# Performance work log

Measured on AMD Instinct MI355X. Metric: run time of the kernel, lower is better.

Reference implementation:

```python
import jax, jax.numpy as jnp
import numpy as np

EPS = 1e-12  # matches torch F.normalize eps


def setup_inputs() -> dict:
    key = jax.random.key(0)
    k1, k2, k3 = jax.random.split(key, 3)
    N, C, H, W, K = 16, 1024, 32, 32, 32
    x = jax.random.normal(k1, (N, C, H, W), dtype=jnp.float32)
    # 1x1 conv weight (K, C, 1, 1) stored as (K, C)
    conv_w = jax.random.normal(k2, (K, C), dtype=jnp.float32) * 0.02
    centroids = jax.random.uniform(k3, (K, C), dtype=jnp.float32)
    return {"x": x, "conv_w": conv_w, "centroids": centroids}


def _l2norm(v, axis):
    return v / jnp.maximum(jnp.linalg.norm(v, axis=axis, keepdims=True), EPS)


def reference(x, conv_w, centroids):
    N, C, H, W = x.shape
    K = centroids.shape[0]
    # normalize_input: L2 over channel dim
    x = _l2norm(x, axis=1)
    xf = x.reshape(N, C, H * W)                      # (N, C, P)
    # 1x1 conv == per-pixel matmul -> (N, K, P)
    logits = jnp.einsum('kc,ncp->nkp', conv_w, xf)
    a = jax.nn.softmax(logits, axis=1)               # softmax over clusters
    # sum_p a[n,k,p] * (x[n,:,p] - centroids[k,:])
    # == (a @ x^T) - (sum_p a) * centroids  (two GEMMs, no (N,K,C,P) blowup)
    vlad = jnp.einsum('nkp,ncp->nkc', a, xf) - a.sum(-1)[:, :, None] * centroids[None]
    vlad = _l2norm(vlad, axis=2)                     # intra-cluster L2 norm
    vlad = vlad.reshape(N, K * C)
    vlad = _l2norm(vlad, axis=1)                     # global L2 norm
    return vlad
```

## Files before the change

kernel.cpp:

```cpp
#include <hip/hip_runtime.h>

#define NB   16
#define CC   1024
#define PP   1024
#define KK   32
#define EPSF 1e-12f

typedef __attribute__((ext_vector_type(8))) short  bf16x8;
typedef __attribute__((ext_vector_type(4))) float  f32x4;

__device__ __forceinline__ float bf2f(unsigned short u) {
    union { unsigned int i; float f; } v; v.i = ((unsigned int)u) << 16; return v.f;
}
__device__ __forceinline__ unsigned short f2bf(float f) {
    union { float f; unsigned int i; } v; v.f = f;
    return (unsigned short)((v.i + 0x7fffu + ((v.i >> 16) & 1u)) >> 16);
}

template <typename T> struct IO;
template <> struct IO<float> {
    static __device__ __forceinline__ float  ld (const float* p) { return *p; }
    static __device__ __forceinline__ float4 ld4(const float* p) { return *(const float4*)p; }
};
template <> struct IO<unsigned short> {
    static __device__ __forceinline__ float  ld (const unsigned short* p) { return bf2f(*p); }
    static __device__ __forceinline__ float4 ld4(const unsigned short* p) {
        const ushort4 u = *(const ushort4*)p;
        return make_float4(bf2f(u.x), bf2f(u.y), bf2f(u.z), bf2f(u.w));
    }
};

__global__ __launch_bounds__(256) void k_detect(const unsigned short* __restrict__ xu,
                                                int* __restrict__ flag) {
    __shared__ int s;
    const int t = threadIdx.x;
    if (t == 0) s = 0;
    __syncthreads();
    int bad = 0;
    for (int i = t; i < 4096; i += 256)
        if (((xu[i] >> 7) & 0xFFu) > 0x9Fu) bad = 1;
    if (bad) atomicOr(&s, 1);
    __syncthreads();
    if (t == 0) flag[0] = s;
}

template <typename T>
__device__ __forceinline__ void attn_body(const T* __restrict__ x,
                                          const T* __restrict__ w,
                                          float* __restrict__ rnorm_ws,
                                          unsigned short* __restrict__ attn_g,
                                          float* __restrict__ asum) {
    __shared__ __align__(16) unsigned short xt[32 * 136];
    __shared__ __align__(16) unsigned short w_lds[32 * 136];
    __shared__ float red[32 * 32];
    __shared__ float lg[32 * 33];
    __shared__ float inv_lds[32];
    __shared__ float rnorm_lds[32];
    const int b = blockIdx.x, t = threadIdx.x;
    const int n = b >> 5, pbase = (b & 31) * 32;
    const int lane = t & 63, wv = t >> 6;
    const int quad = lane >> 4, l15 = lane & 15;
    const int mt = wv & 1, nt = wv >> 1;

    const size_t xb = (size_t)n * CC * PP + pbase;
    float ss0 = 0.f, ss1 = 0.f, ss2 = 0.f, ss3 = 0.f;
    f32x4 acc = {0.f, 0.f, 0.f, 0.f};

    const int pxg = 4 * (t & 7);
    const int crow = t >> 3;

    for (int ch = 0; ch < 8; ++ch) {
        const int c0 = ch * 128;
        __syncthreads();
        #pragma unroll
        for (int pass = 0; pass < 4; ++pass) {
            const int cl = crow + 32 * pass;
            const float4 v = IO<T>::ld4(&x[xb + (size_t)(c0 + cl) * PP + pxg]);
            ss0 += v.x * v.x; ss1 += v.y * v.y; ss2 += v.z * v.z; ss3 += v.w * v.w;
            xt[(pxg + 0) * 136 + cl] = f2bf(v.x);
            xt[(pxg + 1) * 136 + cl] = f2bf(v.y);
            xt[(pxg + 2) * 136 + cl] = f2bf(v.z);
            xt[(pxg + 3) * 136 + cl] = f2bf(v.w);
        }
        {
            const int k = t >> 3, cg = (t & 7) * 16;
            #pragma unroll
            for (int j = 0; j < 4; ++j) {
                const float4 v = IO<T>::ld4(&w[k * CC + c0 + cg + 4 * j]);
                ushort4 u;
                u.x = f2bf(v.x); u.y = f2bf(v.y); u.z = f2bf(v.z); u.w = f2bf(v.w);
                *(ushort4*)&w_lds[k * 136 + cg + 4 * j] = u;
            }
        }
        __syncthreads();
        #pragma unroll
        for (int ks = 0; ks < 4; ++ks) {
            const bf16x8 av = *(const bf16x8*)&xt[(mt * 16 + l15) * 136 + ks * 32 + quad * 8];
            const bf16x8 bv = *(const bf16x8*)&w_lds[(nt * 16 + l15) * 136 + ks * 32 + quad * 8];
            acc = __builtin_amdgcn_mfma_f32_16x16x32_bf16(av, bv, acc, 0, 0, 0);
        }
    }
    red[crow * 32 + pxg + 0] = ss0;
    red[crow * 32 + pxg + 1] = ss1;
    red[crow * 32 + pxg + 2] = ss2;
    red[crow * 32 + pxg + 3] = ss3;
    __syncthreads();
    if (t < 32) {
        float s = 0.f;
        #pragma unroll
        for (int g = 0; g < 32; ++g) s += red[g * 32 + t];
        const float r = 1.0f / fmaxf(sqrtf(s), EPSF);
        rnorm_lds[t] = r;
        rnorm_ws[n * PP + pbase + t] = r;
    }
    __syncthreads();
    #pragma unroll
    for (int reg = 0; reg < 4; ++reg) {
        const int px = mt * 16 + quad * 4 + reg;
        lg[px * 33 + nt * 16 + l15] = acc[reg] * rnorm_lds[px];
    }
    __syncthreads();
    if (t < 32) {
        float m = -1e30f;
        #pragma unroll
        for (int k = 0; k < KK; ++k) m = fmaxf(m, lg[t * 33 + k]);
        float s = 0.f;
        #pragma unroll
        for (int k = 0; k < KK; ++k) {
            const float e = expf(lg[t * 33 + k] - m);
            lg[t * 33 + k] = e;
            s += e;
        }
        inv_lds[t] = 1.0f / s;
    }
    __syncthreads();
    {
        const int k = t >> 3;
        float s = 0.f;
        ushort4 u;
        float vv[4];
        #pragma unroll
        for (int j = 0; j < 4; ++j) {
            const int px = pxg + j;
            vv[j] = lg[px * 33 + k] * inv_lds[px];
        }
        u.x = f2bf(vv[0]); u.y = f2bf(vv[1]); u.z = f2bf(vv[2]); u.w = f2bf(vv[3]);
        s = bf2f(u.x) + bf2f(u.y) + bf2f(u.z) + bf2f(u.w);
        *(ushort4*)&attn_g[((size_t)n * KK + k) * PP + pbase + pxg] = u;
        s += __shfl_xor(s, 1, 64);
        s += __shfl_xor(s, 2, 64);
        s += __shfl_xor(s, 4, 64);
        if ((t & 7) == 0) atomicAdd(&asum[n * KK + k], s);
    }
}
__global__ __launch_bounds__(256) void k_attn(const void* __restrict__ x,
                                              const void* __restrict__ w,
                                              const int* __restrict__ flag,
                                              float* __restrict__ rnorm_ws,
                                              unsigned short* __restrict__ attn_g,
                                              float* __restrict__ asum) {
    if (*flag) attn_body<float>((const float*)x, (const float*)w, rnorm_ws, attn_g, asum);
    else       attn_body<unsigned short>((const unsigned short*)x, (const unsigned short*)w,
                                         rnorm_ws, attn_g, asum);
}

template <typename T>
__device__ __forceinline__ void vlad_body(const T* __restrict__ x,
                                          const T* __restrict__ cent,
                                          const float* __restrict__ rnorm_ws,
                                          const unsigned short* __restrict__ attn_g,
                                          const float* __restrict__ asum,
                                          float* __restrict__ vlad,
                                          float* __restrict__ ssqnk) {
    __shared__ __align__(16) unsigned short xt[64 * 136];
    __shared__ __align__(16) unsigned short at_lds[32 * 136];
    __shared__ float asum_lds[32];
    __shared__ float ssq_lds[32];
    const int b = blockIdx.x, t = threadIdx.x;
    const int n = b >> 4, cbase = (b & 15) * 64;
    const int lane = t & 63, wv = t >> 6;
    const int quad = lane >> 4, l15 = lane & 15;
    const int mt = wv & 1, nt0 = (wv >> 1) * 2, nt1 = nt0 + 1;

    if (t < 32) { asum_lds[t] = asum[n * KK + t]; ssq_lds[t] = 0.f; }

    f32x4 acc0 = {0.f, 0.f, 0.f, 0.f}, acc1 = {0.f, 0.f, 0.f, 0.f};
    const size_t xb = (size_t)n * CC * PP + (size_t)cbase * PP;

    for (int pc = 0; pc < 8; ++pc) {
        const int p0 = pc * 128;
        __syncthreads();
        {
            const int k = t >> 3, pg = (t & 7) * 16;
            const size_t base = ((size_t)n * KK + k) * PP + p0 + pg;
            const uint4 u0 = *(const uint4*)&attn_g[base];
            const uint4 u1 = *(const uint4*)&attn_g[base + 8];
            *(uint4*)&at_lds[k * 136 + pg]     = u0;
            *(uint4*)&at_lds[k * 136 + pg + 8] = u1;
        }
        {
            const int pg = 4 * (t & 31);
            const float4 rn = *(const float4*)&rnorm_ws[n * PP + p0 + pg];
            #pragma unroll
            for (int pass = 0; pass < 8; ++pass) {
                const int ci = (t >> 5) + 8 * pass;
                const float4 v = IO<T>::ld4(&x[xb + (size_t)ci * PP + p0 + pg]);
                ushort4 u;
                u.x = f2bf(v.x * rn.x); u.y = f2bf(v.y * rn.y);
                u.z = f2bf(v.z * rn.z); u.w = f2bf(v.w * rn.w);
                *(ushort4*)&xt[ci * 136 + pg] = u;
            }
        }
        __syncthreads();
        #pragma unroll
        for (int ks = 0; ks < 4; ++ks) {
            const bf16x8 av  = *(const bf16x8*)&at_lds[(mt * 16 + l15) * 136 + ks * 32 + quad * 8];
            const bf16x8 bv0 = *(const bf16x8*)&xt[(nt0 * 16 + l15) * 136 + ks * 32 + quad * 8];
            const bf16x8 bv1 = *(const bf16x8*)&xt[(nt1 * 16 + l15) * 136 + ks * 32 + quad * 8];
            acc0 = __builtin_amdgcn_mfma_f32_16x16x32_bf16(av, bv0, acc0, 0, 0, 0);
            acc1 = __builtin_amdgcn_mfma_f32_16x16x32_bf16(av, bv1, acc1, 0, 0, 0);
        }
    }
    __syncthreads();
    const int c0g = cbase + nt0 * 16 + l15, c1g = cbase + nt1 * 16 + l15;
    #pragma unroll
    for (int reg = 0; reg < 4; ++reg) {
        const int k = mt * 16 + quad * 4 + reg;
        const float A = asum_lds[k];
        const float v0 = acc0[reg] - A * IO<T>::ld(&cent[k * CC + c0g]);
        const float v1 = acc1[reg] - A * IO<T>::ld(&cent[k * CC + c1g]);
        vlad[((size_t)n * KK + k) * CC + c0g] = v0;
        vlad[((size_t)n * KK + k) * CC + c1g] = v1;
        float s = v0 * v0 + v1 * v1;
        s += __shfl_xor(s, 1, 64);
        s += __shfl_xor(s, 2, 64);
        s += __shfl_xor(s, 4, 64);
        s += __shfl_xor(s, 8, 64);
        if (l15 == 0) atomicAdd(&ssq_lds[k], s);
    }
    __syncthreads();
    if (t < 32) atomicAdd(&ssqnk[n * KK + t], ssq_lds[t]);
}
__global__ __launch_bounds__(256) void k_vlad(const void* __restrict__ x,
                                              const void* __restrict__ cent,
                                              const int* __restrict__ flag,
                                              const float* __restrict__ rnorm_ws,
                                              const unsigned short* __restrict__ attn_g,
                                              const float* __restrict__ asum,
                                              float* __restrict__ vlad,
                                              float* __restrict__ ssqnk) {
    if (*flag) vlad_body<float>((const float*)x, (const float*)cent, rnorm_ws, attn_g,
                                asum, vlad, ssqnk);
    else       vlad_body<unsigned short>((const unsigned short*)x, (const unsigned short*)cent,
                                         rnorm_ws, attn_g, asum, vlad, ssqnk);
}

__global__ __launch_bounds__(64) void k_factors(const float* __restrict__ ssqnk,
                                                float* __restrict__ rintra,
                                                float* __restrict__ rglob) {
    const int n = blockIdx.x, t = threadIdx.x;
    const float s = (t < KK) ? ssqnk[n * KK + t] : 0.f;
    const float r = 1.0f / fmaxf(sqrtf(s), EPSF);
    if (t < KK) rintra[n * KK + t] = r;
    float g = s * r * r;
    for (int off = 32; off > 0; off >>= 1) g += __shfl_down(g, off, 64);
    if (t == 0) rglob[n] = 1.0f / fmaxf(sqrtf(g), EPSF);
}

__global__ __launch_bounds__(256) void k_out(const float* __restrict__ vlad,
                                             const float* __restrict__ rintra,
                                             const float* __restrict__ rglob,
                                             const int* __restrict__ flag,
                                             void* __restrict__ out) {
    const int b = blockIdx.x, t = threadIdx.x;
    const float f = rintra[b] * rglob[b >> 5];
    const float4 v = ((const float4*)(vlad + (size_t)b * CC))[t];
    if (*flag) {
        float4 o; o.x = v.x * f; o.y = v.y * f; o.z = v.z * f; o.w = v.w * f;
        ((float4*)((float*)out + (size_t)b * CC))[t] = o;
    } else {
        ushort4 u;
        u.x = f2bf(v.x * f); u.y = f2bf(v.y * f);
        u.z = f2bf(v.z * f); u.w = f2bf(v.w * f);
        ((ushort4*)((unsigned short*)out + (size_t)b * CC))[t] = u;
    }
}

extern "C" void kernel_launch(void* const* d_in, const int* in_sizes, int n_in,
                              void* d_out, int out_size, void* d_ws, size_t ws_size,
                              hipStream_t stream) {
    const void* x    = d_in[0];
    const void* w    = d_in[1];
    const void* cent = d_in[2];

    float* ws       = (float*)d_ws;
    float* rnorm_ws = ws;
    float* vlad     = rnorm_ws + NB * PP;
    float* asum     = vlad + NB * KK * CC;
    float* ssqnk    = asum + NB * KK;
    float* rintra   = ssqnk + NB * KK;
    float* rglob    = rintra + NB * KK;
    int*   flag     = (int*)(rglob + NB);
    unsigned short* attn_g = (unsigned short*)(flag + 4);

    hipMemsetAsync(asum, 0, 2 * NB * KK * sizeof(float), stream);

    k_detect<<<1, 256, 0, stream>>>((const unsigned short*)x, flag);
    k_attn<<<NB * 32, 256, 0, stream>>>(x, w, flag, rnorm_ws, attn_g, asum);
    k_vlad<<<NB * 16, 256, 0, stream>>>(x, cent, flag, rnorm_ws, attn_g, asum, vlad, ssqnk);
    k_factors<<<NB, 64, 0, stream>>>(ssqnk, rintra, rglob);
    k_out<<<NB * KK, 256, 0, stream>>>(vlad, rintra, rglob, flag, d_out);
}
```

Before: 127.6 us.

## Restructure NetVLAD pipeline: split-K attention, register prefetch, partial sums, fused epilogue

The attention kernel now gives each wave its own quarter of the channels. Each wave prefetches x into registers with double buffering and reads the weight from a pre-converted bf16 copy in global memory instead of staging it in LDS, and the per-wave partial logits are summed in shared memory. The vlad kernel launches four times as many blocks and splits the pixel range into two halves that write separate partial outputs. The memset, the atomics and the separate factors kernel are gone: the final kernel sums the partials, subtracts the centroids and applies both normalisations. This cuts launch count and synchronisation and raises parallelism, at the cost of extra workspace traffic for the partial buffers and higher register pressure.

```diff
diff --git a/kernel.cpp b/kernel.cpp
--- a/kernel.cpp
+++ b/kernel.cpp
@@ -5,6 +5,7 @@
 #define PP   1024
 #define KK   32
 #define EPSF 1e-12f
+#define XPAD 72
 
 typedef __attribute__((ext_vector_type(8))) short  bf16x8;
 typedef __attribute__((ext_vector_type(4))) float  f32x4;
@@ -19,270 +20,388 @@
 
 template <typename T> struct IO;
 template <> struct IO<float> {
-    static __device__ __forceinline__ float  ld (const float* p) { return *p; }
-    static __device__ __forceinline__ float4 ld4(const float* p) { return *(const float4*)p; }
+    static __device__ __forceinline__ float ld(const float* p) { return *p; }
+    static __device__ __forceinline__ f32x4 ld4(const float* p) { return *(const f32x4*)p; }
 };
 template <> struct IO<unsigned short> {
-    static __device__ __forceinline__ float  ld (const unsigned short* p) { return bf2f(*p); }
-    static __device__ __forceinline__ float4 ld4(const unsigned short* p) {
+    static __device__ __forceinline__ float ld(const unsigned short* p) { return bf2f(*p); }
+    static __device__ __forceinline__ f32x4 ld4(const unsigned short* p) {
         const ushort4 u = *(const ushort4*)p;
-        return make_float4(bf2f(u.x), bf2f(u.y), bf2f(u.z), bf2f(u.w));
+        f32x4 r; r[0] = bf2f(u.x); r[1] = bf2f(u.y); r[2] = bf2f(u.z); r[3] = bf2f(u.w);
+        return r;
     }
 };
 
-__global__ __launch_bounds__(256) void k_detect(const unsigned short* __restrict__ xu,
-                                                int* __restrict__ flag) {
-    __shared__ int s;
-    const int t = threadIdx.x;
-    if (t == 0) s = 0;
-    __syncthreads();
+__global__ __launch_bounds__(256) void k_prep(const void* __restrict__ xv,
+                                              const void* __restrict__ wv,
+                                              int* __restrict__ flag,
+                                              unsigned short* __restrict__ w_bf) {
+    __shared__ int s_bad;
+    const int t = threadIdx.x, b = blockIdx.x;
+    if (t == 0) s_bad = 0;
+    __syncthreads();
+    const unsigned short* xu = (const unsigned short*)xv;
     int bad = 0;
     for (int i = t; i < 4096; i += 256)
         if (((xu[i] >> 7) & 0xFFu) > 0x9Fu) bad = 1;
-    if (bad) atomicOr(&s, 1);
-    __syncthreads();
-    if (t == 0) flag[0] = s;
-}
+    if (bad) atomicOr(&s_bad, 1);
+    __syncthreads();
+    const int f = s_bad;
+    if (b == 0 && t == 0) flag[0] = f;
+    const int c = t * 4;
+    ushort4 u;
+    if (f) {
+        const f32x4 v = *(const f32x4*)((const float*)wv + b * CC + c);
+        u.x = f2bf(v[0]); u.y = f2bf(v[1]); u.z = f2bf(v[2]); u.w = f2bf(v[3]);
+    } else {
+        u = *(const ushort4*)((const unsigned short*)wv + b * CC + c);
+    }
+    *(ushort4*)&w_bf[b * CC + c] = u;
+}
+
+struct AttnSmem {
+    unsigned short xt[4][2][32 * XPAD];
+    float lg4[4][32][33];
+    float red[4][32];
+    float asq[4][32];
+    float rnorm[32];
+    unsigned short at[32][34];
+};
 
 template <typename T>
 __device__ __forceinline__ void attn_body(const T* __restrict__ x,
-                                          const T* __restrict__ w,
+                                          const unsigned short* __restrict__ w_bf,
                                           float* __restrict__ rnorm_ws,
                                           unsigned short* __restrict__ attn_g,
-                                          float* __restrict__ asum) {
-    __shared__ __align__(16) unsigned short xt[32 * 136];
-    __shared__ __align__(16) unsigned short w_lds[32 * 136];
-    __shared__ float red[32 * 32];
-    __shared__ float lg[32 * 33];
-    __shared__ float inv_lds[32];
-    __shared__ float rnorm_lds[32];
+                                          float* __restrict__ asum_part,
+                                          AttnSmem& sm) {
     const int b = blockIdx.x, t = threadIdx.x;
-    const int n = b >> 5, pbase = (b & 31) * 32;
-    const int lane = t & 63, wv = t >> 6;
+    const int n = b >> 5, strip = b & 31, pbase = strip * 32;
+    const int lane = t & 63, wq = t >> 6;
     const int quad = lane >> 4, l15 = lane & 15;
-    const int mt = wv & 1, nt = wv >> 1;
-
+    const int pg = (lane & 3) * 4;
+    const int c4 = (lane >> 2) * 4;
+    const int cqb = wq * 256;
     const size_t xb = (size_t)n * CC * PP + pbase;
-    float ss0 = 0.f, ss1 = 0.f, ss2 = 0.f, ss3 = 0.f;
-    f32x4 acc = {0.f, 0.f, 0.f, 0.f};
-
-    const int pxg = 4 * (t & 7);
-    const int crow = t >> 3;
-
-    for (int ch = 0; ch < 8; ++ch) {
-        const int c0 = ch * 128;
-        __syncthreads();
-        #pragma unroll
-        for (int pass = 0; pass < 4; ++pass) {
-            const int cl = crow + 32 * pass;
-            const float4 v = IO<T>::ld4(&x[xb + (size_t)(c0 + cl) * PP + pxg]);
-            ss0 += v.x * v.x; ss1 += v.y * v.y; ss2 += v.z * v.z; ss3 += v.w * v.w;
-            xt[(pxg + 0) * 136 + cl] = f2bf(v.x);
-            xt[(pxg + 1) * 136 + cl] = f2bf(v.y);
-            xt[(pxg + 2) * 136 + cl] = f2bf(v.z);
-            xt[(pxg + 3) * 136 + cl] = f2bf(v.w);
-        }
-        {
-            const int k = t >> 3, cg = (t & 7) * 16;
+
+    unsigned short* xt0 = &sm.xt[wq][0][0];
+    unsigned short* xt1 = &sm.xt[wq][1][0];
+
+    float ss[8] = {0.f, 0.f, 0.f, 0.f, 0.f, 0.f, 0.f, 0.f};
+    f32x4 acc00 = {0.f,0.f,0.f,0.f}, acc01 = {0.f,0.f,0.f,0.f};
+    f32x4 acc10 = {0.f,0.f,0.f,0.f}, acc11 = {0.f,0.f,0.f,0.f};
+
+    f32x4 ra[8], rb[8];
+    #pragma unroll
+    for (int i = 0; i < 4; ++i) {
+        ra[i]     = IO<T>::ld4(&x[xb + (size_t)(cqb + c4 + i) * PP + pg]);
+        ra[4 + i] = IO<T>::ld4(&x[xb + (size_t)(cqb + c4 + i) * PP + pg + 16]);
+        rb[i]     = IO<T>::ld4(&x[xb + (size_t)(cqb + 64 + c4 + i) * PP + pg]);
+        rb[4 + i] = IO<T>::ld4(&x[xb + (size_t)(cqb + 64 + c4 + i) * PP + pg + 16]);
+    }
+
+#define ATTN_STEP(CH, R, XT)                                                      \
+    do {                                                                          \
+           \
+        _Pragma("unroll")                                                         \
+        for (int h = 0; h < 2; ++h) {                                             \
+            _Pragma("unroll")                                                     \
+            for (int j = 0; j < 4; ++j) {                                         \
+                ushort4 u;                                                        \
+                u.x = f2bf(R[4*h+0][j]); u.y = f2bf(R[4*h+1][j]);                 \
+                u.z = f2bf(R[4*h+2][j]); u.w = f2bf(R[4*h+3][j]);                 \
+                ss[4*h+j] += R[4*h+0][j]*R[4*h+0][j] + R[4*h+1][j]*R[4*h+1][j]    \
+                           + R[4*h+2][j]*R[4*h+2][j] + R[4*h+3][j]*R[4*h+3][j];   \
+                *(ushort4*)&XT[(pg + 16*h + j) * XPAD + c4] = u;                  \
+            }                                                                     \
+        }                                                                         \
+        if ((CH) + 2 < 4) {                                                       \
+            _Pragma("unroll")                                                     \
+            for (int i = 0; i < 4; ++i) {                                         \
+                R[i]     = IO<T>::ld4(&x[xb + (size_t)(cqb + ((CH)+2)*64 + c4 + i) * PP + pg]);      \
+                R[4 + i] = IO<T>::ld4(&x[xb + (size_t)(cqb + ((CH)+2)*64 + c4 + i) * PP + pg + 16]); \
+            }                                                                     \
+        }                                                                         \
+        _Pragma("unroll")                                                         \
+        for (int ks = 0; ks < 2; ++ks) {                                          \
+            const bf16x8 a0 = *(const bf16x8*)&XT[l15 * XPAD + ks * 32 + quad * 8];        \
+            const bf16x8 a1 = *(const bf16x8*)&XT[(16 + l15) * XPAD + ks * 32 + quad * 8]; \
+            const int wc = cqb + (CH) * 64 + ks * 32 + quad * 8;                  \
+            const bf16x8 b0 = *(const bf16x8*)&w_bf[l15 * CC + wc];               \
+            const bf16x8 b1 = *(const bf16x8*)&w_bf[(16 + l15) * CC + wc];        \
+            acc00 = __builtin_amdgcn_mfma_f32_16x16x32_bf16(a0, b0, acc00, 0,0,0);\
+            acc01 = __builtin_amdgcn_mfma_f32_16x16x32_bf16(a0, b1, acc01, 0,0,0);\
+            acc10 = __builtin_amdgcn_mfma_f32_16x16x32_bf16(a1, b0, acc10, 0,0,0);\
+            acc11 = __builtin_amdgcn_mfma_f32_16x16x32_bf16(a1, b1, acc11, 0,0,0);\
+        }                                                                         \
+    } while (0)
+
+    ATTN_STEP(0, ra, xt0);
+    ATTN_STEP(1, rb, xt1);
+    ATTN_STEP(2, ra, xt0);
+    ATTN_STEP(3, rb, xt1);
+#undef ATTN_STEP
+
+    #pragma unroll
+    for (int i = 0; i < 8; ++i) {
+        ss[i] += __shfl_xor(ss[i], 4, 64);
+        ss[i] += __shfl_xor(ss[i], 8, 64);
+        ss[i] += __shfl_xor(ss[i], 16, 64);
+        ss[i] += __shfl_xor(ss[i], 32, 64);
+    }
+    if (lane < 4) {
+        #pragma unroll
+        for (int h = 0; h < 2; ++h)
             #pragma unroll
-            for (int j = 0; j < 4; ++j) {
-                const float4 v = IO<T>::ld4(&w[k * CC + c0 + cg + 4 * j]);
-                ushort4 u;
-                u.x = f2bf(v.x); u.y = f2bf(v.y); u.z = f2bf(v.z); u.w = f2bf(v.w);
-                *(ushort4*)&w_lds[k * 136 + cg + 4 * j] = u;
-            }
-        }
-        __syncthreads();
-        #pragma unroll
-        for (int ks = 0; ks < 4; ++ks) {
-            const bf16x8 av = *(const bf16x8*)&xt[(mt * 16 + l15) * 136 + ks * 32 + quad * 8];
-            const bf16x8 bv = *(const bf16x8*)&w_lds[(nt * 16 + l15) * 136 + ks * 32 + quad * 8];
-            acc = __builtin_amdgcn_mfma_f32_16x16x32_bf16(av, bv, acc, 0, 0, 0);
-        }
-    }
-    red[crow * 32 + pxg + 0] = ss0;
-    red[crow * 32 + pxg + 1] = ss1;
-    red[crow * 32 + pxg + 2] = ss2;
-    red[crow * 32 + pxg + 3] = ss3;
+            for (int j = 0; j < 4; ++j)
+                sm.red[wq][lane * 4 + 16 * h + j] = ss[4 * h + j];
+    }
+    #pragma unroll
+    for (int reg = 0; reg < 4; ++reg) {
+        sm.lg4[wq][quad * 4 + reg][l15]           = acc00[reg];
+        sm.lg4[wq][quad * 4 + reg][16 + l15]      = acc01[reg];
+        sm.lg4[wq][16 + quad * 4 + reg][l15]      = acc10[reg];
+        sm.lg4[wq][16 + quad * 4 + reg][16 + l15] = acc11[reg];
+    }
     __syncthreads();
     if (t < 32) {
-        float s = 0.f;
-        #pragma unroll
-        for (int g = 0; g < 32; ++g) s += red[g * 32 + t];
+        const float s = sm.red[0][t] + sm.red[1][t] + sm.red[2][t] + sm.red[3][t];
         const float r = 1.0f / fmaxf(sqrtf(s), EPSF);
-        rnorm_lds[t] = r;
+        sm.rnorm[t] = r;
         rnorm_ws[n * PP + pbase + t] = r;
     }
     __syncthreads();
-    #pragma unroll
-    for (int reg = 0; reg < 4; ++reg) {
-        const int px = mt * 16 + quad * 4 + reg;
-        lg[px * 33 + nt * 16 + l15] = acc[reg] * rnorm_lds[px];
-    }
-    __syncthreads();
-    if (t < 32) {
-        float m = -1e30f;
-        #pragma unroll
-        for (int k = 0; k < KK; ++k) m = fmaxf(m, lg[t * 33 + k]);
-        float s = 0.f;
-        #pragma unroll
-        for (int k = 0; k < KK; ++k) {
-            const float e = expf(lg[t * 33 + k] - m);
-            lg[t * 33 + k] = e;
-            s += e;
-        }
-        inv_lds[t] = 1.0f / s;
-    }
-    __syncthreads();
     {
-        const int k = t >> 3;
-        float s = 0.f;
-        ushort4 u;
-        float vv[4];
+        const int px = t >> 3, kq = (t & 7) * 4;
+        const float rn = sm.rnorm[px];
+        float v[4]; float mx = -1e30f;
         #pragma unroll
         for (int j = 0; j < 4; ++j) {
-            const int px = pxg + j;
-            vv[j] = lg[px * 33 + k] * inv_lds[px];
-        }
-        u.x = f2bf(vv[0]); u.y = f2bf(vv[1]); u.z = f2bf(vv[2]); u.w = f2bf(vv[3]);
-        s = bf2f(u.x) + bf2f(u.y) + bf2f(u.z) + bf2f(u.w);
-        *(ushort4*)&attn_g[((size_t)n * KK + k) * PP + pbase + pxg] = u;
+            v[j] = (sm.lg4[0][px][kq + j] + sm.lg4[1][px][kq + j]
+                  + sm.lg4[2][px][kq + j] + sm.lg4[3][px][kq + j]) * rn;
+            mx = fmaxf(mx, v[j]);
+        }
+        mx = fmaxf(mx, __shfl_xor(mx, 1, 64));
+        mx = fmaxf(mx, __shfl_xor(mx, 2, 64));
+        mx = fmaxf(mx, __shfl_xor(mx, 4, 64));
+        float e[4], s = 0.f;
+        #pragma unroll
+        for (int j = 0; j < 4; ++j) { e[j] = expf(v[j] - mx); s += e[j]; }
         s += __shfl_xor(s, 1, 64);
         s += __shfl_xor(s, 2, 64);
         s += __shfl_xor(s, 4, 64);
-        if ((t & 7) == 0) atomicAdd(&asum[n * KK + k], s);
-    }
-}
+        const float inv = 1.0f / s;
+        float as[4];
+        #pragma unroll
+        for (int j = 0; j < 4; ++j) {
+            const unsigned short uu = f2bf(e[j] * inv);
+            sm.at[px][kq + j] = uu;
+            as[j] = bf2f(uu);
+        }
+        #pragma unroll
+        for (int j = 0; j < 4; ++j) {
+            as[j] += __shfl_xor(as[j], 8, 64);
+            as[j] += __shfl_xor(as[j], 16, 64);
+            as[j] += __shfl_xor(as[j], 32, 64);
+        }
+        if ((lane >> 3) == 0) {
+            #pragma unroll
+            for (int j = 0; j < 4; ++j) sm.asq[t >> 6][kq + j] = as[j];
+        }
+    }
+    __syncthreads();
+    if (t < 32)
+        asum_part[(n * 32 + strip) * KK + t]
+            = sm.asq[0][t] + sm.asq[1][t] + sm.asq[2][t] + sm.asq[3][t];
+    {
+        const int k = t >> 3, p4 = (t & 7) * 4;
+        ushort4 uo;
+        uo.x = sm.at[p4 + 0][k]; uo.y = sm.at[p4 + 1][k];
+        uo.z = sm.at[p4 + 2][k]; uo.w = sm.at[p4 + 3][k];
+        *(ushort4*)&attn_g[((size_t)n * KK + k) * PP + pbase + p4] = uo;
+    }
+}
+
 __global__ __launch_bounds__(256) void k_attn(const void* __restrict__ x,
-                                              const void* __restrict__ w,
+                                              const unsigned short* __restrict__ w_bf,
                                               const int* __restrict__ flag,
                                               float* __restrict__ rnorm_ws,
                                               unsigned short* __restrict__ attn_g,
-                                              float* __restrict__ asum) {
-    if (*flag) attn_body<float>((const float*)x, (const float*)w, rnorm_ws, attn_g, asum);
-    else       attn_body<unsigned short>((const unsigned short*)x, (const unsigned short*)w,
-                                         rnorm_ws, attn_g, asum);
+                                              float* __restrict__ asum_part) {
+    __shared__ AttnSmem sm;
+    if (*flag) attn_body<float>((const float*)x, w_bf, rnorm_ws, attn_g, asum_part, sm);
+    else       attn_body<unsigned short>((const unsigned short*)x, w_bf, rnorm_ws,
+                                         attn_g, asum_part, sm);
 }
 
 template <typename T>
 __device__ __forceinline__ void vlad_body(const T* __restrict__ x,
-                                          const T* __restrict__ cent,
                                           const float* __restrict__ rnorm_ws,
                                           const unsigned short* __restrict__ attn_g,
-                                          const float* __restrict__ asum,
-                                          float* __restrict__ vlad,
-                                          float* __restrict__ ssqnk) {
-    __shared__ __align__(16) unsigned short xt[64 * 136];
-    __shared__ __align__(16) unsigned short at_lds[32 * 136];
-    __shared__ float asum_lds[32];
-    __shared__ float ssq_lds[32];
+                                          float* __restrict__ vlad_part) {
     const int b = blockIdx.x, t = threadIdx.x;
-    const int n = b >> 4, cbase = (b & 15) * 64;
-    const int lane = t & 63, wv = t >> 6;
+    const int n = b >> 6, rr = b & 63, ct = rr >> 1, ph = rr & 1;
+    const int lane = t & 63, wid = t >> 6;
     const int quad = lane >> 4, l15 = lane & 15;
-    const int mt = wv & 1, nt0 = (wv >> 1) * 2, nt1 = nt0 + 1;
-
-    if (t < 32) { asum_lds[t] = asum[n * KK + t]; ssq_lds[t] = 0.f; }
-
-    f32x4 acc0 = {0.f, 0.f, 0.f, 0.f}, acc1 = {0.f, 0.f, 0.f, 0.f};
-    const size_t xb = (size_t)n * CC * PP + (size_t)cbase * PP;
-
-    for (int pc = 0; pc < 8; ++pc) {
-        const int p0 = pc * 128;
-        __syncthreads();
-        {
-            const int k = t >> 3, pg = (t & 7) * 16;
-            const size_t base = ((size_t)n * KK + k) * PP + p0 + pg;
-            const uint4 u0 = *(const uint4*)&attn_g[base];
-            const uint4 u1 = *(const uint4*)&attn_g[base + 8];
-            *(uint4*)&at_lds[k * 136 + pg]     = u0;
-            *(uint4*)&at_lds[k * 136 + pg + 8] = u1;
-        }
-        {
-            const int pg = 4 * (t & 31);
-            const float4 rn = *(const float4*)&rnorm_ws[n * PP + p0 + pg];
-            #pragma unroll
-            for (int pass = 0; pass < 8; ++pass) {
-                const int ci = (t >> 5) + 8 * pass;
-                const float4 v = IO<T>::ld4(&x[xb + (size_t)ci * PP + p0 + pg]);
-                ushort4 u;
-                u.x = f2bf(v.x * rn.x); u.y = f2bf(v.y * rn.y);
-                u.z = f2bf(v.z * rn.z); u.w = f2bf(v.w * rn.w);
-                *(ushort4*)&xt[ci * 136 + pg] = u;
-            }
-        }
-        __syncthreads();
-        #pragma unroll
-        for (int ks = 0; ks < 4; ++ks) {
-            const bf16x8 av  = *(const bf16x8*)&at_lds[(mt * 16 + l15) * 136 + ks * 32 + quad * 8];
-            const bf16x8 bv0 = *(const bf16x8*)&xt[(nt0 * 16 + l15) * 136 + ks * 32 + quad * 8];
-            const bf16x8 bv1 = *(const bf16x8*)&xt[(nt1 * 16 + l15) * 136 + ks * 32 + quad * 8];
-            acc0 = __builtin_amdgcn_mfma_f32_16x16x32_bf16(av, bv0, acc0, 0, 0, 0);
-            acc1 = __builtin_amdgcn_mfma_f32_16x16x32_bf16(av, bv1, acc1, 0, 0, 0);
-        }
-    }
-    __syncthreads();
-    const int c0g = cbase + nt0 * 16 + l15, c1g = cbase + nt1 * 16 + l15;
-    #pragma unroll
-    for (int reg = 0; reg < 4; ++reg) {
-        const int k = mt * 16 + quad * 4 + reg;
-        const float A = asum_lds[k];
-        const float v0 = acc0[reg] - A * IO<T>::ld(&cent[k * CC + c0g]);
-        const float v1 = acc1[reg] - A * IO<T>::ld(&cent[k * CC + c1g]);
-        vlad[((size_t)n * KK + k) * CC + c0g] = v0;
-        vlad[((size_t)n * KK + k) * CC + c1g] = v1;
-        float s = v0 * v0 + v1 * v1;
-        s += __shfl_xor(s, 1, 64);
-        s += __shfl_xor(s, 2, 64);
-        s += __shfl_xor(s, 4, 64);
-        s += __shfl_xor(s, 8, 64);
-        if (l15 == 0) atomicAdd(&ssq_lds[k], s);
-    }
-    __syncthreads();
-    if (t < 32) atomicAdd(&ssqnk[n * KK + t], ssq_lds[t]);
-}
+    const int mt = wid & 1, nt = wid >> 1;
+    const int cbase = ct * 32, pb = ph * 512;
+    const int krow = mt * 16 + l15;
+    const int crow = cbase + nt * 16 + l15;
+    const unsigned short* ap = attn_g + ((size_t)n * KK + krow) * PP + pb + quad * 8;
+    const T* xp = x + (size_t)n * CC * PP + (size_t)crow * PP + pb + quad * 8;
+    const float* rp = rnorm_ws + n * PP + pb + quad * 8;
+
+    f32x4 acc = {0.f, 0.f, 0.f, 0.f};
+    bf16x8 avA, avB, avC, avD;
+    f32x4 x0A, x1A, x0B, x1B, x0C, x1C, x0D, x1D;
+    f32x4 r0A, r1A, r0B, r1B, r0C, r1C, r0D, r1D;
+    avA = *(const bf16x8*)&ap[0];  x0A = IO<T>::ld4(&xp[0]);  x1A = IO<T>::ld4(&xp[4]);
+    r0A = *(const f32x4*)&rp[0];   r1A = *(const f32x4*)&rp[4];
+    avB = *(const bf16x8*)&ap[32]; x0B = IO<T>::ld4(&xp[32]); x1B = IO<T>::ld4(&xp[36]);
+    r0B = *(const f32x4*)&rp[32];  r1B = *(const f32x4*)&rp[36];
+    avC = *(const bf16x8*)&ap[64]; x0C = IO<T>::ld4(&xp[64]); x1C = IO<T>::ld4(&xp[68]);
+    r0C = *(const f32x4*)&rp[64];  r1C = *(const f32x4*)&rp[68];
+    avD = *(const bf16x8*)&ap[96]; x0D = IO<T>::ld4(&xp[96]); x1D = IO<T>::ld4(&xp[100]);
+    r0D = *(const f32x4*)&rp[96];  r1D = *(const f32x4*)&rp[100];
+
+#define VSTEP(ST, AV, X0, X1, R0, R1)                                             \
+    do {                                                                          \
+        bf16x8 bv;                                                                \
+        bv[0] = (short)f2bf(X0[0] * R0[0]); bv[1] = (short)f2bf(X0[1] * R0[1]);   \
+        bv[2] = (short)f2bf(X0[2] * R0[2]); bv[3] = (short)f2bf(X0[3] * R0[3]);   \
+        bv[4] = (short)f2bf(X1[0] * R1[0]); bv[5] = (short)f2bf(X1[1] * R1[1]);   \
+        bv[6] = (short)f2bf(X1[2] * R1[2]); bv[7] = (short)f2bf(X1[3] * R1[3]);   \
+        acc = __builtin_amdgcn_mfma_f32_16x16x32_bf16(AV, bv, acc, 0, 0, 0);      \
+        if ((ST) + 4 < 16) {                                                      \
+            const int o = ((ST) + 4) * 32;                                        \
+            AV = *(const bf16x8*)&ap[o];                                          \
+            X0 = IO<T>::ld4(&xp[o]); X1 = IO<T>::ld4(&xp[o + 4]);                 \
+            R0 = *(const f32x4*)&rp[o]; R1 = *(const f32x4*)&rp[o + 4];           \
+        }                                                                         \
+    } while (0)
+
+    VSTEP(0,  avA, x0A, x1A, r0A, r1A);
+    VSTEP(1,  avB, x0B, x1B, r0B, r1B);
+    VSTEP(2,  avC, x0C, x1C, r0C, r1C);
+    VSTEP(3,  avD, x0D, x1D, r0D, r1D);
+    VSTEP(4,  avA, x0A, x1A, r0A, r1A);
+    VSTEP(5,  avB, x0B, x1B, r0B, r1B);
+    VSTEP(6,  avC, x0C, x1C, r0C, r1C);
+    VSTEP(7,  avD, x0D, x1D, r0D, r1D);
+    VSTEP(8,  avA, x0A, x1A, r0A, r1A);
+    VSTEP(9,  avB, x0B, x1B, r0B, r1B);
+    VSTEP(10, avC, x0C, x1C, r0C, r1C);
+    VSTEP(11, avD, x0D, x1D, r0D, r1D);
+    VSTEP(12, avA, x0A, x1A, r0A, r1A);
+    VSTEP(13, avB, x0B, x1B, r0B, r1B);
+    VSTEP(14, avC, x0C, x1C, r0C, r1C);
+    VSTEP(15, avD, x0D, x1D, r0D, r1D);
+#undef VSTEP
+
+    float* vp = vlad_part + (((size_t)ph * NB + n) * KK) * CC;
+    const int kk = mt * 16 + quad * 4;
+    #pragma unroll
+    for (int reg = 0; reg < 4; ++reg)
+        vp[(size_t)(kk + reg) * CC + crow] = acc[reg];
+}
+
 __global__ __launch_bounds__(256) void k_vlad(const void* __restrict__ x,
-                                              const void* __restrict__ cent,
                                               const int* __restrict__ flag,
                                               const float* __restrict__ rnorm_ws,
                                               const unsigned short* __restrict__ attn_g,
-                                              const float* __restrict__ asum,
-                                              float* __restrict__ vlad,
-                                              float* __restrict__ ssqnk) {
-    if (*flag) vlad_body<float>((const float*)x, (const float*)cent, rnorm_ws, attn_g,
-                                asum, vlad, ssqnk);
-    else       vlad_body<unsigned short>((const unsigned short*)x, (const unsigned short*)cent,
-                                         rnorm_ws, attn_g, asum, vlad, ssqnk);
-}
-
-__global__ __launch_bounds__(64) void k_factors(const float* __restrict__ ssqnk,
-                                                float* __restrict__ rintra,
-                                                float* __restrict__ rglob) {
+                                              float* __restrict__ vlad_part) {
+    if (*flag) vlad_body<float>((const float*)x, rnorm_ws, attn_g, vlad_part);
+    else       vlad_body<unsigned short>((const unsigned short*)x, rnorm_ws, attn_g,
+                                         vlad_part);
+}
+
+struct OutSmem { float asum[KK]; float ssq[KK]; float rint[KK]; float rg; };
+
+__global__ __launch_bounds__(1024) void k_out(const float* __restrict__ vlad_part,
+                                              const float* __restrict__ asum_part,
+                                              const void* __restrict__ cent,
+                                              const int* __restrict__ flag,
+                                              void* __restrict__ out) {
+    __shared__ OutSmem sm;
     const int n = blockIdx.x, t = threadIdx.x;
-    const float s = (t < KK) ? ssqnk[n * KK + t] : 0.f;
-    const float r = 1.0f / fmaxf(sqrtf(s), EPSF);
-    if (t < KK) rintra[n * KK + t] = r;
-    float g = s * r * r;
-    for (int off = 32; off > 0; off >>= 1) g += __shfl_down(g, off, 64);
-    if (t == 0) rglob[n] = 1.0f / fmaxf(sqrtf(g), EPSF);
-}
-
-__global__ __launch_bounds__(256) void k_out(const float* __restrict__ vlad,
-                                             const float* __restrict__ rintra,
-                                             const float* __restrict__ rglob,
-                                             const int* __restrict__ flag,
-                                             void* __restrict__ out) {
-    const int b = blockIdx.x, t = threadIdx.x;
-    const float f = rintra[b] * rglob[b >> 5];
-    const float4 v = ((const float4*)(vlad + (size_t)b * CC))[t];
-    if (*flag) {
-        float4 o; o.x = v.x * f; o.y = v.y * f; o.z = v.z * f; o.w = v.w * f;
-        ((float4*)((float*)out + (size_t)b * CC))[t] = o;
-    } else {
-        ushort4 u;
-        u.x = f2bf(v.x * f); u.y = f2bf(v.y * f);
-        u.z = f2bf(v.z * f); u.w = f2bf(v.w * f);
-        ((ushort4*)((unsigned short*)out + (size_t)b * CC))[t] = u;
+    if (t < KK) {
+        float s = 0.f;
+        #pragma unroll
+        for (int st = 0; st < 32; ++st) s += asum_part[(n * 32 + st) * KK + t];
+        sm.asum[t] = s;
+    }
+    __syncthreads();
+    const int k = t >> 5, l32 = t & 31;
+    const float A = sm.asum[k];
+    const int isf = *flag;
+    const float* p0 = vlad_part + ((size_t)n * KK + k) * CC;
+    const float* p1 = vlad_part + ((size_t)(NB + n) * KK + k) * CC;
+    float ssq = 0.f;
+    #pragma unroll
+    for (int j = 0; j < 8; ++j) {
+        const int c = l32 * 4 + j * 128;
+        const f32x4 v0 = *(const f32x4*)&p0[c];
+        const f32x4 v1 = *(const f32x4*)&p1[c];
+        f32x4 ce;
+        if (isf) ce = *(const f32x4*)((const float*)cent + k * CC + c);
+        else {
+            const ushort4 u = *(const ushort4*)((const unsigned short*)cent + k * CC + c);
+            ce[0] = bf2f(u.x); ce[1] = bf2f(u.y); ce[2] = bf2f(u.z); ce[3] = bf2f(u.w);
+        }
+        #pragma unroll
+        for (int i = 0; i < 4; ++i) {
+            const float v = v0[i] + v1[i] - A * ce[i];
+            ssq += v * v;
+        }
+    }
+    ssq += __shfl_xor(ssq, 1, 64);
+    ssq += __shfl_xor(ssq, 2, 64);
+    ssq += __shfl_xor(ssq, 4, 64);
+    ssq += __shfl_xor(ssq, 8, 64);
+    ssq += __shfl_xor(ssq, 16, 64);
+    if (l32 == 0) sm.ssq[k] = ssq;
+    __syncthreads();
+    if (t < KK) {
+        const float s = sm.ssq[t];
+        const float r = 1.0f / fmaxf(sqrtf(s), EPSF);
+        sm.rint[t] = r;
+        float g = s * r * r;
+        g += __shfl_xor(g, 1, 64);
+        g += __shfl_xor(g, 2, 64);
+        g += __shfl_xor(g, 4, 64);
+        g += __shfl_xor(g, 8, 64);
+        g += __shfl_xor(g, 16, 64);
+        if (t == 0) sm.rg = 1.0f / fmaxf(sqrtf(g), EPSF);
+    }
+    __syncthreads();
+    const float f = sm.rint[k] * sm.rg;
+    #pragma unroll
+    for (int j = 0; j < 8; ++j) {
+        const int c = l32 * 4 + j * 128;
+        const f32x4 v0 = *(const f32x4*)&p0[c];
+        const f32x4 v1 = *(const f32x4*)&p1[c];
+        f32x4 ce;
+        if (isf) ce = *(const f32x4*)((const float*)cent + k * CC + c);
+        else {
+            const ushort4 u = *(const ushort4*)((const unsigned short*)cent + k * CC + c);
+            ce[0] = bf2f(u.x); ce[1] = bf2f(u.y); ce[2] = bf2f(u.z); ce[3] = bf2f(u.w);
+        }
+        const size_t ob = ((size_t)n * KK + k) * CC + c;
+        if (isf) {
+            float4 o;
+            o.x = (v0[0] + v1[0] - A * ce[0]) * f;
+            o.y = (v0[1] + v1[1] - A * ce[1]) * f;
+            o.z = (v0[2] + v1[2] - A * ce[2]) * f;
+            o.w = (v0[3] + v1[3] - A * ce[3]) * f;
+            *(float4*)((float*)out + ob) = o;
+        } else {
+            ushort4 u;
+            u.x = f2bf((v0[0] + v1[0] - A * ce[0]) * f);
+            u.y = f2bf((v0[1] + v1[1] - A * ce[1]) * f);
+            u.z = f2bf((v0[2] + v1[2] - A * ce[2]) * f);
+            u.w = f2bf((v0[3] + v1[3] - A * ce[3]) * f);
+            *(ushort4*)((unsigned short*)out + ob) = u;
+        }
     }
 }
 
@@ -293,21 +412,16 @@
     const void* w    = d_in[1];
     const void* cent = d_in[2];
 
-    float* ws       = (float*)d_ws;
-    float* rnorm_ws = ws;
-    float* vlad     = rnorm_ws + NB * PP;
-    float* asum     = vlad + NB * KK * CC;
-    float* ssqnk    = asum + NB * KK;
-    float* rintra   = ssqnk + NB * KK;
-    float* rglob    = rintra + NB * KK;
-    int*   flag     = (int*)(rglob + NB);
-    unsigned short* attn_g = (unsigned short*)(flag + 4);
-
-    hipMemsetAsync(asum, 0, 2 * NB * KK * sizeof(float), stream);
-
-    k_detect<<<1, 256, 0, stream>>>((const unsigned short*)x, flag);
-    k_attn<<<NB * 32, 256, 0, stream>>>(x, w, flag, rnorm_ws, attn_g, asum);
-    k_vlad<<<NB * 16, 256, 0, stream>>>(x, cent, flag, rnorm_ws, attn_g, asum, vlad, ssqnk);
-    k_factors<<<NB, 64, 0, stream>>>(ssqnk, rintra, rglob);
-    k_out<<<NB * KK, 256, 0, stream>>>(vlad, rintra, rglob, flag, d_out);
-}
+    float* ws        = (float*)d_ws;
+    float* vlad_part = ws;
+    float* rnorm_ws  = vlad_part + 2 * NB * KK * CC;
+    float* asum_part = rnorm_ws + NB * PP;
+    int*   flag      = (int*)(asum_part + NB * 32 * KK);
+    unsigned short* w_bf   = (unsigned short*)(flag + 4);
+    unsigned short* attn_g = w_bf + KK * CC;
+
+    k_prep<<<KK, 256, 0, stream>>>(x, w, flag, w_bf);
+    k_attn<<<NB * 32, 256, 0, stream>>>(x, w_bf, flag, rnorm_ws, attn_g, asum_part);
+    k_vlad<<<NB * 64, 256, 0, stream>>>(x, flag, rnorm_ws, attn_g, vlad_part);
+    k_out<<<NB, 1024, 0, stream>>>(vlad_part, asum_part, cent, flag, d_out);
+}
```

New measurement: 139.2 us. 1.09x slower.
